# Performance work log

Hardware: AMD Instinct MI355X
Metric: run time of the kernel (lower is better)

Reference implementation:

```python
import jax, jax.numpy as jnp
import numpy as np

B, S, H = 8, 4096, 2048
DH = 64            # selector hidden dim
K = 256            # num_perturb_tokens (min(K, S) = 256)
SCALE = 0.1        # perturbation_scale
FIXED_TYPE = 1     # type_values[1] == 0.0
TYPE_VALUES = jnp.array([-1.0, 0.0, 1.0], dtype=jnp.float32)


def setup_inputs() -> dict:
    key = jax.random.key(0)
    k_hs, k_u, k_w1, k_w2 = jax.random.split(key, 4)
    hidden_states = jax.random.normal(k_hs, (B, S, H), dtype=jnp.float32)
    # torch.rand_like -> uniform [0,1); keep strictly >0 so -log(-log(u)) is finite
    noise_u = jax.random.uniform(k_u, (B, S), dtype=jnp.float32, minval=1e-9, maxval=1.0)
    w1 = jax.random.normal(k_w1, (H, DH), dtype=jnp.float32) * 0.02
    b1 = jnp.zeros((DH,), dtype=jnp.float32)
    w2 = jax.random.normal(k_w2, (DH, 1), dtype=jnp.float32) * 0.02
    b2 = jnp.zeros((1,), dtype=jnp.float32)
    return {"hidden_states": hidden_states, "noise_u": noise_u,
            "w1": w1, "b1": b1, "w2": w2, "b2": b2}


def reference(hidden_states, noise_u, w1, b1, w2, b2):
    hs = hidden_states.astype(jnp.float32)                       # (B,S,H)
    # TokenSelectorNetwork: Linear -> ReLU -> Linear -> squeeze(-1)
    h = jax.nn.relu(jnp.einsum('bsh,hd->bsd', hs, w1) + b1)       # (B,S,DH)
    selection_logits = (jnp.einsum('bsd,do->bso', h, w2) + b2)[..., 0]  # (B,S)

    # gumbel-perturbed top-k token selection (deterministic=False path)
    gumbel = -jnp.log(-jnp.log(noise_u))
    _, selected_indices = jax.lax.top_k(selection_logits + gumbel, K)   # (B,K)

    # log prob of selection (gather from log-softmax, mean over K)
    log_probs_all = jax.nn.log_softmax(selection_logits, axis=-1)       # (B,S)
    log_prob = jnp.take_along_axis(log_probs_all, selected_indices, axis=1).mean(axis=-1)  # (B,)

    # fixed perturbation type -> constant perturb values, scattered over selected rows
    perturb_types = jnp.full((B, K), FIXED_TYPE, dtype=jnp.int32)
    perturb_values = TYPE_VALUES[perturb_types] * SCALE                 # (B,K), all zeros here
    expanded_values = jnp.broadcast_to(perturb_values[..., None], (B, K, H))
    sel_clamped = jnp.clip(selected_indices, 0, S - 1)
    batch_idx = jnp.arange(B)[:, None]                                  # (B,1)
    perturbed = hs.at[batch_idx, sel_clamped].set(expanded_values)      # scatter_ along dim 1

    return (perturbed.astype(jnp.float16), selected_indices, perturb_types, log_prob)
```

## Files before the change

### kernel.cpp

```cpp
#include <hip/hip_runtime.h>
#include <hip/hip_fp16.h>

#define NB 8
#define NS 4096
#define NH 2048
#define NDH 64
#define NK 256
#define BK 32
#define MT 128
#define KS 4
#define KCH (NH / KS)

__global__ __launch_bounds__(512) void k_sel_gemm(
    const float* __restrict__ hs, const float* __restrict__ w1,
    float* __restrict__ out0, float* __restrict__ part)
{
    __shared__ float As[MT][BK + 4];
    __shared__ float Ws[BK][NDH];

    const int tid = threadIdx.x;
    const int tx = tid & 7;
    const int ty = tid >> 3;
    const int tile = blockIdx.x & 255;
    const int kc = blockIdx.x >> 8;
    const int tokenBase = tile * MT;
    const int kBase = kc * KCH;

    const int sK = (tid & 7) * 4;
    const long long aBase = (long long)(tokenBase + ty) * NH + kBase + sK;
    const int wRow = tid >> 4;
    const int wCol = (tid & 15) * 4;
    const float* wBase = w1 + (long long)(kBase + wRow) * NDH + wCol;

    float acc[2][8];
#pragma unroll
    for (int t = 0; t < 2; ++t)
#pragma unroll
        for (int j = 0; j < 8; ++j) acc[t][j] = 0.0f;

    float4 va[2], wv;
#pragma unroll
    for (int r = 0; r < 2; ++r)
        va[r] = *reinterpret_cast<const float4*>(hs + aBase + (long long)r * 64 * NH);
    wv = *reinterpret_cast<const float4*>(wBase);

    for (int ko = 0; ko < KCH; ko += BK) {
#pragma unroll
        for (int r = 0; r < 2; ++r)
            *reinterpret_cast<float4*>(&As[ty + r * 64][sK]) = va[r];
        *reinterpret_cast<float4*>(&Ws[wRow][wCol]) = wv;
        __syncthreads();

#pragma unroll
        for (int r = 0; r < 2; ++r) {
            float4 o;
            o.x = __half2float(__float2half(va[r].x));
            o.y = __half2float(__float2half(va[r].y));
            o.z = __half2float(__float2half(va[r].z));
            o.w = __half2float(__float2half(va[r].w));
            *reinterpret_cast<float4*>(out0 + aBase + ko + (long long)r * 64 * NH) = o;
        }
        if (ko + BK < KCH) {
#pragma unroll
            for (int r = 0; r < 2; ++r)
                va[r] = *reinterpret_cast<const float4*>(
                    hs + aBase + (ko + BK) + (long long)r * 64 * NH);
            wv = *reinterpret_cast<const float4*>(wBase + (long long)(ko + BK) * NDH);
        }

#pragma unroll
        for (int kk = 0; kk < BK; kk += 4) {
            float4 av[2];
#pragma unroll
            for (int t = 0; t < 2; ++t)
                av[t] = *reinterpret_cast<const float4*>(&As[ty + 64 * t][kk]);
#pragma unroll
            for (int i = 0; i < 4; ++i) {
                const float4 w0 = *reinterpret_cast<const float4*>(&Ws[kk + i][tx * 8]);
                const float4 w1v = *reinterpret_cast<const float4*>(&Ws[kk + i][tx * 8 + 4]);
#pragma unroll
                for (int t = 0; t < 2; ++t) {
                    const float a = reinterpret_cast<const float*>(&av[t])[i];
                    acc[t][0] += a * w0.x;  acc[t][1] += a * w0.y;
                    acc[t][2] += a * w0.z;  acc[t][3] += a * w0.w;
                    acc[t][4] += a * w1v.x; acc[t][5] += a * w1v.y;
                    acc[t][6] += a * w1v.z; acc[t][7] += a * w1v.w;
                }
            }
        }
        __syncthreads();
    }

#pragma unroll
    for (int t = 0; t < 2; ++t) {
        const long long o =
            ((long long)kc * (NB * NS) + tokenBase + ty + 64 * t) * NDH + tx * 8;
        *reinterpret_cast<float4*>(part + o) =
            make_float4(acc[t][0], acc[t][1], acc[t][2], acc[t][3]);
        *reinterpret_cast<float4*>(part + o + 4) =
            make_float4(acc[t][4], acc[t][5], acc[t][6], acc[t][7]);
    }
}

__global__ __launch_bounds__(256) void k_reduce(
    const float* __restrict__ part, const float* __restrict__ b1,
    const float* __restrict__ w2, const float* __restrict__ b2,
    float* __restrict__ logits)
{
    const int T = blockIdx.x * 4 + (threadIdx.x >> 6);
    const int lane = threadIdx.x & 63;
    float s = 0.0f;
#pragma unroll
    for (int kc = 0; kc < KS; ++kc)
        s += part[((long long)kc * (NB * NS) + T) * NDH + lane];
    const float h = fmaxf(s + b1[lane], 0.0f);
    float p = h * w2[lane];
#pragma unroll
    for (int m = 1; m < 64; m <<= 1) p += __shfl_xor(p, m, 64);
    if (lane == 0) logits[T] = p + b2[0];
}

__global__ __launch_bounds__(256) void k_topk(
    const float* __restrict__ logits, const float* __restrict__ noise,
    float* __restrict__ outIdx, float* __restrict__ outType,
    float* __restrict__ outLP, int* __restrict__ wsIdx)
{
    __shared__ unsigned int ukey[NS];
    __shared__ float rawl[NS];
    __shared__ unsigned int hist[256];
    __shared__ unsigned int candU[512];
    __shared__ int candIdx[512];
    __shared__ int sel[NK];
    __shared__ float redw[4];
    __shared__ unsigned int misc[3];

    const int b = blockIdx.x;
    const int tid = threadIdx.x;
    const int lane = tid & 63;
    const int wid = tid >> 6;

    for (int e = tid; e < NS; e += 256) {
        const float l = logits[b * NS + e];
        const float u = noise[b * NS + e];
        const float g = -logf(-logf(u));
        unsigned int x = __float_as_uint(l + g);
        x = (x & 0x80000000u) ? ~x : (x | 0x80000000u);
        ukey[e] = x;
        rawl[e] = l;
    }
    if (tid == 0) { misc[0] = 0u; misc[1] = NK; misc[2] = 0u; }
    __syncthreads();

    for (int pass = 0; pass < 4; ++pass) {
        const int shift = 24 - pass * 8;
        hist[tid] = 0u;
        __syncthreads();
        const unsigned int pfx = misc[0];
        const unsigned int rem = misc[1];
        for (int e = tid; e < NS; e += 256) {
            const unsigned int x = ukey[e];
            if (pass == 0 || (x >> (shift + 8)) == pfx)
                atomicAdd(&hist[(x >> shift) & 255u], 1u);
        }
        __syncthreads();
        if (tid < 64) {
            const unsigned int h0 = hist[4 * tid];
            const unsigned int h1 = hist[4 * tid + 1];
            const unsigned int h2 = hist[4 * tid + 2];
            const unsigned int h3 = hist[4 * tid + 3];
            const unsigned int g = h0 + h1 + h2 + h3;
            unsigned int s = g;
#pragma unroll
            for (int m = 1; m < 64; m <<= 1) {
                const unsigned int v = __shfl_down(s, m, 64);
                if (tid + m < 64) s += v;
            }
            const unsigned int Snext = s - g;
            const unsigned int s3 = Snext + h3;
            const unsigned int s2 = s3 + h2;
            const unsigned int s1 = s2 + h1;
            const unsigned int s0 = s1 + h0;
            const unsigned int ge[4] = { s0, s1, s2, s3 };
            const unsigned int gt[4] = { s1, s2, s3, Snext };
#pragma unroll
            for (int i = 0; i < 4; ++i) {
                if (ge[i] >= rem && gt[i] < rem) {
                    misc[0] = (pfx << 8) | (unsigned int)(4 * tid + i);
                    misc[1] = rem - gt[i];
                }
            }
        }
        __syncthreads();
    }

    const unsigned int T = misc[0];
    for (int e = tid; e < NS; e += 256) {
        if (ukey[e] >= T) {
            const unsigned int slot = atomicAdd(&misc[2], 1u);
            if (slot < 512u) { candU[slot] = ukey[e]; candIdx[slot] = e; }
        }
    }
    __syncthreads();
    const int C = (int)min(misc[2], 512u);

    for (int c = tid; c < C; c += 256) {
        const unsigned int xu = candU[c];
        const int xi = candIdx[c];
        int r = 0;
        for (int j = 0; j < C; ++j) {
            const unsigned int yu = candU[j];
            r += (int)((yu > xu) || (yu == xu && candIdx[j] < xi));
        }
        if (r < NK) {
            outIdx[b * NK + r] = (float)xi;
            outType[b * NK + r] = 1.0f;
            wsIdx[b * NK + r] = xi;
            sel[r] = xi;
        }
    }

    float lm = -INFINITY;
    for (int e = tid; e < NS; e += 256) lm = fmaxf(lm, rawl[e]);
#pragma unroll
    for (int m = 32; m; m >>= 1) lm = fmaxf(lm, __shfl_xor(lm, m, 64));
    if (lane == 0) redw[wid] = lm;
    __syncthreads();
    const float maxv = fmaxf(fmaxf(redw[0], redw[1]), fmaxf(redw[2], redw[3]));
    __syncthreads();
    float ls = 0.0f;
    for (int e = tid; e < NS; e += 256) ls += expf(rawl[e] - maxv);
#pragma unroll
    for (int m = 32; m; m >>= 1) ls += __shfl_xor(ls, m, 64);
    if (lane == 0) redw[wid] = ls;
    __syncthreads();
    const float lse = logf(redw[0] + redw[1] + redw[2] + redw[3]);
    __syncthreads();
    float contrib = rawl[sel[tid]] - maxv - lse;
#pragma unroll
    for (int m = 32; m; m >>= 1) contrib += __shfl_xor(contrib, m, 64);
    if (lane == 0) redw[wid] = contrib;
    __syncthreads();
    if (tid == 0) outLP[b] = (redw[0] + redw[1] + redw[2] + redw[3]) / (float)NK;
}

__global__ __launch_bounds__(256) void k_zero_rows(
    const int* __restrict__ wsIdx, float* __restrict__ out0)
{
    const int blk = blockIdx.x;
    const int b = blk >> 8;
    const int r = blk & 255;
    const int row = wsIdx[b * NK + r];
    const float4 z = make_float4(0.f, 0.f, 0.f, 0.f);
    float4* p = reinterpret_cast<float4*>(out0 + ((long long)(b * NS + row)) * NH);
    p[threadIdx.x]       = z;
    p[threadIdx.x + 256] = z;
}

extern "C" void kernel_launch(void* const* d_in, const int* in_sizes, int n_in,
                              void* d_out, int out_size, void* d_ws, size_t ws_size,
                              hipStream_t stream) {
    const float* hs    = (const float*)d_in[0];
    const float* noise = (const float*)d_in[1];
    const float* w1    = (const float*)d_in[2];
    const float* b1    = (const float*)d_in[3];
    const float* w2    = (const float*)d_in[4];
    const float* b2    = (const float*)d_in[5];

    float* out0    = (float*)d_out;
    float* outIdx  = out0 + (long long)NB * NS * NH;
    float* outType = outIdx + NB * NK;
    float* outLP   = outType + NB * NK;

    float* logits = (float*)d_ws;
    int*   wsIdx  = (int*)d_ws + NB * NS;
    float* part   = (float*)d_ws + NB * NS + NB * NK;

    k_sel_gemm<<<256 * KS, 512, 0, stream>>>(hs, w1, out0, part);
    k_reduce<<<NB * NS / 4, 256, 0, stream>>>(part, b1, w2, b2, logits);
    k_topk<<<NB, 256, 0, stream>>>(logits, noise, outIdx, outType, outLP, wsIdx);
    k_zero_rows<<<NB * NK, 256, 0, stream>>>(wsIdx, out0);
}
```

Before: 514.8 us.

## Rewrite selector GEMM as per-lane token rows with scalar-broadcast weights

Replaces the LDS-tiled GEMM with a register-only scheme. Each lane owns one token row and reads it straight from global memory, and each wave computes 32 of the 64 hidden outputs using weights at a wave-uniform address, so the weights can go through scalar loads. This removes the shared-memory staging and the barriers. The cost is uncoalesced row-strided activation loads, since adjacent lanes are 8KB apart, and each row is read twice by the two wave halves. Stores of the half-precision copy are split between those two halves.

```diff
diff --git a/kernel.cpp b/kernel.cpp
--- a/kernel.cpp
+++ b/kernel.cpp
@@ -6,99 +6,70 @@
 #define NH 2048
 #define NDH 64
 #define NK 256
-#define BK 32
-#define MT 128
 #define KS 4
 #define KCH (NH / KS)
 
-__global__ __launch_bounds__(512) void k_sel_gemm(
+__global__ __launch_bounds__(256) void k_sel_gemm(
     const float* __restrict__ hs, const float* __restrict__ w1,
     float* __restrict__ out0, float* __restrict__ part)
 {
-    __shared__ float As[MT][BK + 4];
-    __shared__ float Ws[BK][NDH];
-
-    const int tid = threadIdx.x;
-    const int tx = tid & 7;
-    const int ty = tid >> 3;
+    const int tid  = threadIdx.x;
+    const int lane = tid & 63;
+    const int w    = tid >> 6;
+    const int tsub = w & 1;
+    const int dhH  = w >> 1;
+
     const int tile = blockIdx.x & 255;
-    const int kc = blockIdx.x >> 8;
-    const int tokenBase = tile * MT;
-    const int kBase = kc * KCH;
-
-    const int sK = (tid & 7) * 4;
-    const long long aBase = (long long)(tokenBase + ty) * NH + kBase + sK;
-    const int wRow = tid >> 4;
-    const int wCol = (tid & 15) * 4;
-    const float* wBase = w1 + (long long)(kBase + wRow) * NDH + wCol;
-
-    float acc[2][8];
-#pragma unroll
-    for (int t = 0; t < 2; ++t)
-#pragma unroll
-        for (int j = 0; j < 8; ++j) acc[t][j] = 0.0f;
-
-    float4 va[2], wv;
-#pragma unroll
-    for (int r = 0; r < 2; ++r)
-        va[r] = *reinterpret_cast<const float4*>(hs + aBase + (long long)r * 64 * NH);
-    wv = *reinterpret_cast<const float4*>(wBase);
-
-    for (int ko = 0; ko < KCH; ko += BK) {
-#pragma unroll
-        for (int r = 0; r < 2; ++r)
-            *reinterpret_cast<float4*>(&As[ty + r * 64][sK]) = va[r];
-        *reinterpret_cast<float4*>(&Ws[wRow][wCol]) = wv;
-        __syncthreads();
-
-#pragma unroll
-        for (int r = 0; r < 2; ++r) {
-            float4 o;
-            o.x = __half2float(__float2half(va[r].x));
-            o.y = __half2float(__float2half(va[r].y));
-            o.z = __half2float(__float2half(va[r].z));
-            o.w = __half2float(__float2half(va[r].w));
-            *reinterpret_cast<float4*>(out0 + aBase + ko + (long long)r * 64 * NH) = o;
-        }
-        if (ko + BK < KCH) {
-#pragma unroll
-            for (int r = 0; r < 2; ++r)
-                va[r] = *reinterpret_cast<const float4*>(
-                    hs + aBase + (ko + BK) + (long long)r * 64 * NH);
-            wv = *reinterpret_cast<const float4*>(wBase + (long long)(ko + BK) * NDH);
-        }
-
-#pragma unroll
-        for (int kk = 0; kk < BK; kk += 4) {
-            float4 av[2];
-#pragma unroll
-            for (int t = 0; t < 2; ++t)
-                av[t] = *reinterpret_cast<const float4*>(&As[ty + 64 * t][kk]);
-#pragma unroll
-            for (int i = 0; i < 4; ++i) {
-                const float4 w0 = *reinterpret_cast<const float4*>(&Ws[kk + i][tx * 8]);
-                const float4 w1v = *reinterpret_cast<const float4*>(&Ws[kk + i][tx * 8 + 4]);
-#pragma unroll
-                for (int t = 0; t < 2; ++t) {
-                    const float a = reinterpret_cast<const float*>(&av[t])[i];
-                    acc[t][0] += a * w0.x;  acc[t][1] += a * w0.y;
-                    acc[t][2] += a * w0.z;  acc[t][3] += a * w0.w;
-                    acc[t][4] += a * w1v.x; acc[t][5] += a * w1v.y;
-                    acc[t][6] += a * w1v.z; acc[t][7] += a * w1v.w;
-                }
-            }
-        }
-        __syncthreads();
-    }
-
-#pragma unroll
-    for (int t = 0; t < 2; ++t) {
-        const long long o =
-            ((long long)kc * (NB * NS) + tokenBase + ty + 64 * t) * NDH + tx * 8;
-        *reinterpret_cast<float4*>(part + o) =
-            make_float4(acc[t][0], acc[t][1], acc[t][2], acc[t][3]);
-        *reinterpret_cast<float4*>(part + o + 4) =
-            make_float4(acc[t][4], acc[t][5], acc[t][6], acc[t][7]);
+    const int kc   = blockIdx.x >> 8;
+
+    const int token = tile * 128 + tsub * 64 + lane;
+    const long long rowOff = (long long)token * NH + (long long)kc * KCH;
+    const float* arow = hs + rowOff;
+    float*       orow = out0 + rowOff;
+
+    const int dhOff = __builtin_amdgcn_readfirstlane(dhH * 32);
+    const float* wbase = w1 + (long long)kc * KCH * NDH + dhOff;
+
+    float acc[32];
+#pragma unroll
+    for (int j = 0; j < 32; ++j) acc[j] = 0.0f;
+
+    const int storeLo = (dhH == 0) ? 0 : (KCH / 2);
+    const int storeHi = storeLo + KCH / 2;
+
+    for (int k0 = 0; k0 < KCH; k0 += 8) {
+        const float4 a0 = *reinterpret_cast<const float4*>(arow + k0);
+        const float4 a1 = *reinterpret_cast<const float4*>(arow + k0 + 4);
+
+        if (k0 >= storeLo && k0 < storeHi) {
+            float4 o0, o1;
+            o0.x = __half2float(__float2half(a0.x));
+            o0.y = __half2float(__float2half(a0.y));
+            o0.z = __half2float(__float2half(a0.z));
+            o0.w = __half2float(__float2half(a0.w));
+            o1.x = __half2float(__float2half(a1.x));
+            o1.y = __half2float(__float2half(a1.y));
+            o1.z = __half2float(__float2half(a1.z));
+            o1.w = __half2float(__float2half(a1.w));
+            *reinterpret_cast<float4*>(orow + k0)     = o0;
+            *reinterpret_cast<float4*>(orow + k0 + 4) = o1;
+        }
+
+        const float av[8] = { a0.x, a0.y, a0.z, a0.w, a1.x, a1.y, a1.z, a1.w };
+#pragma unroll
+        for (int kk = 0; kk < 8; ++kk) {
+            const float a = av[kk];
+            const float* wr = wbase + (long long)(k0 + kk) * NDH;
+#pragma unroll
+            for (int j = 0; j < 32; ++j) acc[j] += a * wr[j];
+        }
+    }
+
+    const long long o = ((long long)kc * (NB * NS) + token) * NDH + dhOff;
+#pragma unroll
+    for (int j = 0; j < 32; j += 4) {
+        *reinterpret_cast<float4*>(part + o + j) =
+            make_float4(acc[j], acc[j + 1], acc[j + 2], acc[j + 3]);
     }
 }
 
@@ -275,7 +246,7 @@
     int*   wsIdx  = (int*)d_ws + NB * NS;
     float* part   = (float*)d_ws + NB * NS + NB * NK;
 
-    k_sel_gemm<<<256 * KS, 512, 0, stream>>>(hs, w1, out0, part);
+    k_sel_gemm<<<256 * KS, 256, 0, stream>>>(hs, w1, out0, part);
     k_reduce<<<NB * NS / 4, 256, 0, stream>>>(part, b1, w2, b2, logits);
     k_topk<<<NB, 256, 0, stream>>>(logits, noise, outIdx, outType, outLP, wsIdx);
     k_zero_rows<<<NB * NK, 256, 0, stream>>>(wsIdx, out0);
```

New measurement: 734.7 us. 1.43x slower.
